# Performance work log

Measured on AMD Instinct MI355X. Metric: run time of the kernel, lower is better.

Reference implementation:

```python
import jax, jax.numpy as jnp
import numpy as np

HEAD_DIM = 64
N_HEADS = 32
N_KV_HEADS = 8
ROPE_THETA = 10000.0


def _rotate_half(x):
    h = x.shape[-1] // 2
    return jnp.concatenate([-x[..., h:], x[..., :h]], axis=-1)


def _rope_cos_sin(position_ids, head_dim, theta, dtype):
    # position_ids: [b, s] int
    inv_freq = 1.0 / (theta ** (jnp.arange(0, head_dim, 2, dtype=jnp.float32) / head_dim))
    freqs = position_ids.astype(jnp.float32)[..., None] * inv_freq  # [b, s, hd/2]
    emb = jnp.concatenate([freqs, freqs], axis=-1)                  # [b, s, hd]
    return jnp.cos(emb).astype(dtype), jnp.sin(emb).astype(dtype)


def setup_inputs() -> dict:
    key = jax.random.key(0)
    ks = jax.random.split(key, 5)
    B, S, H = 2, 2048, 2048
    KVD = N_KV_HEADS * HEAD_DIM
    x = jax.random.normal(ks[0], (B, S, H), dtype=jnp.float32)
    position_ids = jnp.broadcast_to(jnp.arange(S, dtype=jnp.int64), (B, S))
    # additive causal mask: 0 on/below diagonal, -1e9 above
    causal = jnp.triu(jnp.full((S, S), -1e9, dtype=jnp.float32), k=1)
    mask = causal[None, None, :, :]
    sc = 1.0 / np.sqrt(H)
    wq = jax.random.normal(ks[1], (H, H), dtype=jnp.float32) * sc
    wk = jax.random.normal(ks[2], (KVD, H), dtype=jnp.float32) * sc
    wv = jax.random.normal(ks[3], (KVD, H), dtype=jnp.float32) * sc
    wo = jax.random.normal(ks[4], (H, H), dtype=jnp.float32) * sc
    return {"x": x, "position_ids": position_ids, "mask": mask,
            "wq": wq, "wk": wk, "wv": wv, "wo": wo}


def reference(x, position_ids, mask, wq, wk, wv, wo):
    b, s, h = x.shape
    kv_groups = N_HEADS // N_KV_HEADS
    # projections (Linear with weight [out, in])
    xq = jnp.einsum('bsh,oh->bso', x, wq)
    xk = jnp.einsum('bsh,oh->bso', x, wk)
    xv = jnp.einsum('bsh,oh->bso', x, wv)
    q = xq.reshape(b, s, N_HEADS, HEAD_DIM).transpose(0, 2, 1, 3)      # [b,H,s,d]
    k = xk.reshape(b, s, N_KV_HEADS, HEAD_DIM).transpose(0, 2, 1, 3)   # [b,Hk,s,d]
    v = xv.reshape(b, s, N_KV_HEADS, HEAD_DIM).transpose(0, 2, 1, 3)
    cos, sin = _rope_cos_sin(position_ids, HEAD_DIM, ROPE_THETA, x.dtype)
    cos = cos[:, None, :, :]  # [b,1,s,d]
    sin = sin[:, None, :, :]
    q = q * cos + _rotate_half(q) * sin
    k = k * cos + _rotate_half(k) * sin
    # GQA expand
    k = jnp.repeat(k, kv_groups, axis=1)  # [b,H,s,d]
    v = jnp.repeat(v, kv_groups, axis=1)
    scale = 1.0 / np.sqrt(HEAD_DIM)
    attn = jnp.einsum('bhqd,bhkd->bhqk', q, k) * scale
    attn = attn + mask[:, :, :s, :s]
    attn = jax.nn.softmax(attn.astype(jnp.float32), axis=-1).astype(q.dtype)
    out = jnp.einsum('bhqk,bhkd->bhqd', attn, v)        # [b,H,s,d]
    out = out.transpose(0, 2, 1, 3).reshape(b, s, h)
    return jnp.einsum('bsh,oh->bso', out, wo)
```

## Files before the change

kernel.cpp:

```cpp
#include <hip/hip_runtime.h>

typedef __bf16 bf16;
typedef __bf16 bf16x4 __attribute__((ext_vector_type(4)));
typedef __bf16 bf16x8 __attribute__((ext_vector_type(8)));
typedef float f32x4 __attribute__((ext_vector_type(4)));

#define MFMA16(a, b, c) __builtin_amdgcn_mfma_f32_16x16x32_bf16(a, b, c, 0, 0, 0)

__device__ inline bf16x8 cvt8(const float* __restrict__ p) {
  float4 f0 = ((const float4*)p)[0];
  float4 f1 = ((const float4*)p)[1];
  bf16x8 v;
  v[0] = (bf16)f0.x; v[1] = (bf16)f0.y; v[2] = (bf16)f0.z; v[3] = (bf16)f0.w;
  v[4] = (bf16)f1.x; v[5] = (bf16)f1.y; v[6] = (bf16)f1.z; v[7] = (bf16)f1.w;
  return v;
}

__device__ inline void gl_lds16(const bf16* g, bf16* l) {
  __builtin_amdgcn_global_load_lds(
      (const __attribute__((address_space(1))) unsigned int*)g,
      (__attribute__((address_space(3))) unsigned int*)l, 16, 0, 0);
}

__global__ void detect_kernel(const unsigned* __restrict__ mask,
                              int* __restrict__ flag) {
  *flag = (mask[0] != 0u) ? 1 : 0;
}

__global__ __launch_bounds__(256) void convert_kernel(
    const void* __restrict__ s0, bf16* __restrict__ d0, int n0,
    const void* __restrict__ s1, bf16* __restrict__ d1, int n1,
    const void* __restrict__ s2, bf16* __restrict__ d2, int n2,
    const void* __restrict__ s3, bf16* __restrict__ d3, int n3,
    const int* __restrict__ flag) {
  const int isb = *flag;
  const int c0 = n0 >> 3, c1 = c0 + (n1 >> 3), c2 = c1 + (n2 >> 3);
  const int total = c2 + (n3 >> 3);
  for (int c = blockIdx.x * 256 + threadIdx.x; c < total;
       c += gridDim.x * 256) {
    const void* s; bf16* d; int off;
    if (c < c0)      { s = s0; d = d0; off = c; }
    else if (c < c1) { s = s1; d = d1; off = c - c0; }
    else if (c < c2) { s = s2; d = d2; off = c - c1; }
    else             { s = s3; d = d3; off = c - c2; }
    if (isb) ((uint4*)d)[off] = ((const uint4*)s)[off];
    else     ((bf16x8*)d)[off] = cvt8((const float*)s + (size_t)off * 8);
  }
}

template <int MODE>
__global__ __launch_bounds__(256) void gemm_bt(
    const bf16* __restrict__ Ab, const bf16* __restrict__ Wq,
    const bf16* __restrict__ Wk, const bf16* __restrict__ Wv,
    void* __restrict__ O0, bf16* __restrict__ O1, bf16* __restrict__ O2,
    const int* __restrict__ flag) {
  const int K = 2048;
  __shared__ __align__(16) bf16 As[128 * 32];
  __shared__ __align__(16) bf16 Bs[128 * 32];

  const int m0 = blockIdx.x * 128;
  const int n0 = blockIdx.y * 128;

  const bf16* W;
  int nw0;
  if (MODE == 0) {
    if (n0 < 2048) { W = Wq; nw0 = n0; }
    else if (n0 < 2560) { W = Wk; nw0 = n0 - 2048; }
    else { W = Wv; nw0 = n0 - 2560; }
  } else {
    W = Wq; nw0 = n0;
  }

  const int t = threadIdx.x;
  const int w = t >> 6, lane = t & 63, quad = lane >> 4, l15 = lane & 15;
  const int wm = (w >> 1) * 64, wn = (w & 1) * 64;

  const int ca = t, cb = t + 256;
  const bf16* ga0 = Ab + (size_t)(m0 + (ca >> 2)) * K + (ca & 3) * 8;
  const bf16* ga1 = Ab + (size_t)(m0 + (cb >> 2)) * K + (cb & 3) * 8;
  const bf16* gb0 = W + (size_t)(nw0 + (ca >> 2)) * K + (ca & 3) * 8;
  const bf16* gb1 = W + (size_t)(nw0 + (cb >> 2)) * K + (cb & 3) * 8;
  bf16* lA0 = &As[w * 512];
  bf16* lA1 = &As[2048 + w * 512];
  bf16* lB0 = &Bs[w * 512];
  bf16* lB1 = &Bs[2048 + w * 512];

  f32x4 acc[4][4] = {};

  for (int k0 = 0; k0 < K; k0 += 32) {
    __syncthreads();
    gl_lds16(ga0 + k0, lA0);
    gl_lds16(ga1 + k0, lA1);
    gl_lds16(gb0 + k0, lB0);
    gl_lds16(gb1 + k0, lB1);
    __syncthreads();

    bf16x8 a[4], b[4];
#pragma unroll
    for (int i = 0; i < 4; i++)
      a[i] = *(const bf16x8*)&As[(wm + i * 16 + l15) * 32 + quad * 8];
#pragma unroll
    for (int j = 0; j < 4; j++)
      b[j] = *(const bf16x8*)&Bs[(wn + j * 16 + l15) * 32 + quad * 8];
#pragma unroll
    for (int i = 0; i < 4; i++)
#pragma unroll
      for (int j = 0; j < 4; j++)
        acc[i][j] = MFMA16(a[i], b[j], acc[i][j]);
  }

  if (MODE == 0 && n0 >= 2560) {
#pragma unroll
    for (int i = 0; i < 4; i++)
#pragma unroll
      for (int j = 0; j < 4; j++) {
        int m = m0 + wm + i * 16 + quad * 4;
        int n = (n0 - 2560) + wn + j * 16 + l15;
        int hh = n >> 6, d = n & 63;
        int b_ = m >> 11, s = m & 2047;
        bf16x4 pv;
#pragma unroll
        for (int r = 0; r < 4; r++) pv[r] = (bf16)acc[i][j][r];
        *(bf16x4*)&O2[(((size_t)b_ * 8 + hh) * 64 + d) * 2048 + s] = pv;
      }
    return;
  }
  const int isb = (MODE == 1) ? *flag : 0;
#pragma unroll
  for (int i = 0; i < 4; i++)
#pragma unroll
    for (int j = 0; j < 4; j++)
#pragma unroll
      for (int r = 0; r < 4; r++) {
        int m = m0 + wm + i * 16 + quad * 4 + r;
        int n = n0 + wn + j * 16 + l15;
        float fv = acc[i][j][r];
        if (MODE == 1) {
          if (isb) ((bf16*)O0)[(size_t)m * 2048 + n] = (bf16)fv;
          else     ((float*)O0)[(size_t)m * 2048 + n] = fv;
        } else {
          bf16 bv = (bf16)fv;
          int b_ = m >> 11, s = m & 2047;
          if (n < 2048) {
            int h = n >> 6, d = n & 63;
            ((bf16*)O0)[(((size_t)b_ * 32 + h) * 2048 + s) * 64 + d] = bv;
          } else {
            int nn = n - 2048, h = nn >> 6, d = nn & 63;
            O1[(((size_t)b_ * 8 + h) * 2048 + s) * 64 + d] = bv;
          }
        }
      }
}

__global__ __launch_bounds__(256) void rope_table_kernel(float2* __restrict__ tab) {
  int i = blockIdx.x * 256 + threadIdx.x;
  int s = i >> 5, fi = i & 31;
  float inv = 1.0f / powf(10000.0f, (float)(2 * fi) / 64.0f);
  float fr = (float)s * inv;
  tab[i] = make_float2(cosf(fr), sinf(fr));
}

__global__ __launch_bounds__(256) void rope_kernel(bf16* __restrict__ qb,
                                                   bf16* __restrict__ kb,
                                                   const float2* __restrict__ tab,
                                                   const int* __restrict__ flag) {
  const int QROWS = 2 * 32 * 2048;
  const int isb = *flag;
  int row = blockIdx.x * 8 + (threadIdx.x >> 5);
  int d = threadIdx.x & 31;
  bf16* base = (row < QROWS) ? qb + (size_t)row * 64
                             : kb + (size_t)(row - QROWS) * 64;
  int s = row & 2047;
  float2 cs = tab[s * 32 + d];
  float cb = cs.x, sb = cs.y;
  if (isb) { cb = (float)(bf16)cb; sb = (float)(bf16)sb; }
  float v0 = (float)base[d], v1 = (float)base[d + 32];
  base[d]      = (bf16)(v0 * cb - v1 * sb);
  base[d + 32] = (bf16)(v1 * cb + v0 * sb);
}

__global__ __launch_bounds__(256) void flash_kernel(
    const bf16* __restrict__ qb, const bf16* __restrict__ kb,
    const bf16* __restrict__ vb, bf16* __restrict__ ao) {
  __shared__ __align__(16) bf16 Ks[64 * 64];
  __shared__ __align__(16) bf16 Vt[64 * 72];
  __shared__ __align__(16) bf16 Ps[4][16 * 72];

  const int bx = blockIdx.x;
  const int h = blockIdx.y;
  const int b = blockIdx.z;
  const int kvh = h >> 2;
  const int t = threadIdx.x, w = t >> 6, lane = t & 63;
  const int quad = lane >> 4, l15 = lane & 15;

  const bf16* kg = kb + ((size_t)b * 8 + kvh) * 2048 * 64;
  const bf16* vg = vb + ((size_t)b * 8 + kvh) * 64 * 2048;

  const int vd = t >> 3;
  const int vs = (t & 7) * 8;

#pragma unroll 1
  for (int ti = 0; ti < 2; ti++) {
    const int q0 = (ti == 0 ? bx : 31 - bx) * 64;
    const bf16* qg = qb + (((size_t)b * 32 + h) * 2048 + q0) * 64;

    __syncthreads();
#pragma unroll
    for (int i = 0; i < 2; i++) {
      int c = t + i * 256;
      int row = c >> 3, slot = c & 7;
      *(uint4*)&Ks[row * 64 + ((slot ^ (row & 7)) << 3)] = ((const uint4*)qg)[c];
    }
    __syncthreads();
    const int qrow = w * 16 + l15;
    bf16x8 aq0 = *(const bf16x8*)&Ks[qrow * 64 + ((quad ^ (qrow & 7)) << 3)];
    bf16x8 aq1 = *(const bf16x8*)&Ks[qrow * 64 + (((4 + quad) ^ (qrow & 7)) << 3)];

    f32x4 Oacc[4] = {};
    float m_sm = -1e30f, l_sm = 0.0f;

    const int nk = q0 + 64;
    const int qmax = q0 + w * 16 + 15;
    const int qr_sm = q0 + w * 16 + l15;

    uint4 kr0 = ((const uint4*)kg)[t];
    uint4 kr1 = ((const uint4*)kg)[t + 256];
    uint4 vr0 = *(const uint4*)(vg + (size_t)vd * 2048 + vs);
    uint4 vr1 = *(const uint4*)(vg + (size_t)(vd + 32) * 2048 + vs);

    for (int k0 = 0; k0 < nk; k0 += 64) {
      __syncthreads();
      {
        int row = t >> 3, slot = t & 7;
        *(uint4*)&Ks[row * 64 + ((slot ^ (row & 7)) << 3)] = kr0;
        int row1 = row + 32;
        *(uint4*)&Ks[row1 * 64 + ((slot ^ (row1 & 7)) << 3)] = kr1;
      }
      *(uint4*)&Vt[vd * 72 + vs] = vr0;
      *(uint4*)&Vt[(vd + 32) * 72 + vs] = vr1;
      __syncthreads();

      if (k0 + 64 < nk) {
        const bf16* kn = kg + (size_t)(k0 + 64) * 64;
        kr0 = ((const uint4*)kn)[t];
        kr1 = ((const uint4*)kn)[t + 256];
        vr0 = *(const uint4*)(vg + (size_t)vd * 2048 + (k0 + 64) + vs);
        vr1 = *(const uint4*)(vg + (size_t)(vd + 32) * 2048 + (k0 + 64) + vs);
      }

      f32x4 sf[4] = {};
#pragma unroll
      for (int sub = 0; sub < 4; sub++) {
        if (k0 + sub * 16 <= qmax) {
          int rr = sub * 16 + l15;
          bf16x8 bk0 = *(const bf16x8*)&Ks[rr * 64 + ((quad ^ (rr & 7)) << 3)];
          bf16x8 bk1 = *(const bf16x8*)&Ks[rr * 64 + (((4 + quad) ^ (rr & 7)) << 3)];
          sf[sub] = MFMA16(bk0, aq0, sf[sub]);
          sf[sub] = MFMA16(bk1, aq1, sf[sub]);
        }
      }

#pragma unroll
      for (int sub = 0; sub < 4; sub++) {
        int kk = k0 + sub * 16 + quad * 4;
#pragma unroll
        for (int r = 0; r < 4; r++) {
          float v = sf[sub][r] * 0.125f;
          sf[sub][r] = (kk + r > qr_sm) ? -1e30f : v;
        }
      }

      float mx;
      {
        f32x4 t4;
#pragma unroll
        for (int r = 0; r < 4; r++)
          t4[r] = fmaxf(fmaxf(sf[0][r], sf[1][r]), fmaxf(sf[2][r], sf[3][r]));
        mx = fmaxf(fmaxf(t4[0], t4[1]), fmaxf(t4[2], t4[3]));
      }
      mx = fmaxf(mx, __shfl_xor(mx, 16));
      mx = fmaxf(mx, __shfl_xor(mx, 32));

      float mnew = fmaxf(m_sm, mx);
      float alpha_sm = __expf(m_sm - mnew);
      m_sm = mnew;

#pragma unroll
      for (int sub = 0; sub < 4; sub++)
#pragma unroll
        for (int r = 0; r < 4; r++) sf[sub][r] = __expf(sf[sub][r] - mnew);

      float rs;
      {
        f32x4 t4;
#pragma unroll
        for (int r = 0; r < 4; r++)
          t4[r] = (sf[0][r] + sf[1][r]) + (sf[2][r] + sf[3][r]);
        rs = (t4[0] + t4[1]) + (t4[2] + t4[3]);
      }
      rs += __shfl_xor(rs, 16);
      rs += __shfl_xor(rs, 32);
      l_sm = alpha_sm * l_sm + rs;

      f32x4 alpha_pv;
#pragma unroll
      for (int r = 0; r < 4; r++) alpha_pv[r] = __shfl(alpha_sm, quad * 4 + r);
#pragma unroll
      for (int tt = 0; tt < 4; tt++)
#pragma unroll
        for (int r = 0; r < 4; r++) Oacc[tt][r] *= alpha_pv[r];

#pragma unroll
      for (int sub = 0; sub < 4; sub++) {
        bf16x4 pk;
#pragma unroll
        for (int r = 0; r < 4; r++) pk[r] = (bf16)sf[sub][r];
        *(bf16x4*)&Ps[w][l15 * 72 + sub * 16 + quad * 4] = pk;
      }
      asm volatile("s_waitcnt lgkmcnt(0)" ::: "memory");
      __builtin_amdgcn_sched_barrier(0);

      bf16x8 ap0 = *(const bf16x8*)&Ps[w][l15 * 72 + quad * 8];
#pragma unroll
      for (int tt = 0; tt < 4; tt++) {
        bf16x8 bv = *(const bf16x8*)&Vt[(tt * 16 + l15) * 72 + quad * 8];
        Oacc[tt] = MFMA16(ap0, bv, Oacc[tt]);
      }
      if (k0 + 32 <= qmax) {
        bf16x8 ap1 = *(const bf16x8*)&Ps[w][l15 * 72 + 32 + quad * 8];
#pragma unroll
        for (int tt = 0; tt < 4; tt++) {
          bf16x8 bv = *(const bf16x8*)&Vt[(tt * 16 + l15) * 72 + 32 + quad * 8];
          Oacc[tt] = MFMA16(ap1, bv, Oacc[tt]);
        }
      }
    }

    f32x4 lv;
#pragma unroll
    for (int r = 0; r < 4; r++) lv[r] = __shfl(l_sm, quad * 4 + r);
#pragma unroll
    for (int tt = 0; tt < 4; tt++)
#pragma unroll
      for (int r = 0; r < 4; r++) {
        int m = q0 + w * 16 + quad * 4 + r;
        ao[((size_t)b * 2048 + m) * 2048 + h * 64 + tt * 16 + l15] =
            (bf16)(Oacc[tt][r] / lv[r]);
      }
  }
}

extern "C" void kernel_launch(void* const* d_in, const int* in_sizes, int n_in,
                              void* d_out, int out_size, void* d_ws,
                              size_t ws_size, hipStream_t stream) {
  const void* x = d_in[0];
  const unsigned* maskw = (const unsigned*)d_in[2];
  const void* wq = d_in[3];
  const void* wk = d_in[4];
  const void* wv = d_in[5];
  const void* wo = d_in[6];

  char* ws = (char*)d_ws;
  bf16* qbuf  = (bf16*)(ws);
  bf16* kbuf  = (bf16*)(ws + 16777216);
  bf16* vbuf  = (bf16*)(ws + 20971520);
  bf16* wob   = (bf16*)(ws + 16777216);
  bf16* aobuf = (bf16*)(ws + 25165824);
  bf16* xb    = (bf16*)(ws + 25165824);
  int* flag   = (int*)(ws + 41943040);
  bf16* wqb   = (bf16*)(ws + 41943104);
  bf16* wkb   = (bf16*)(ws + 50331712);
  bf16* wvb   = (bf16*)(ws + 52428864);
  float2* rtab = (float2*)(ws + 54526016);

  detect_kernel<<<1, 1, 0, stream>>>(maskw, flag);
  rope_table_kernel<<<256, 256, 0, stream>>>(rtab);
  convert_kernel<<<2048, 256, 0, stream>>>(x, xb, 8388608, wq, wqb, 4194304,
                                           wk, wkb, 1048576, wv, wvb, 1048576,
                                           flag);
  gemm_bt<0><<<dim3(32, 24), 256, 0, stream>>>(xb, wqb, wkb, wvb, qbuf, kbuf,
                                               vbuf, flag);
  rope_kernel<<<20480, 256, 0, stream>>>(qbuf, kbuf, rtab, flag);
  flash_kernel<<<dim3(16, 32, 2), 256, 0, stream>>>(qbuf, kbuf, vbuf, aobuf);
  convert_kernel<<<2048, 256, 0, stream>>>(wo, wob, 4194304, nullptr, nullptr,
                                           0, nullptr, nullptr, 0, nullptr,
                                           nullptr, 0, flag);
  gemm_bt<1><<<dim3(32, 16), 256, 0, stream>>>(aobuf, wob, nullptr, nullptr,
                                               d_out, nullptr, nullptr, flag);
}
```

Before: 357.9 us.

## Fuse RoPE into QKV GEMM epilogue and add lazy rescaling to flash softmax

```diff
diff --git a/kernel.cpp b/kernel.cpp
--- a/kernel.cpp
+++ b/kernel.cpp
@@ -6,6 +6,7 @@
 typedef float f32x4 __attribute__((ext_vector_type(4)));
 
 #define MFMA16(a, b, c) __builtin_amdgcn_mfma_f32_16x16x32_bf16(a, b, c, 0, 0, 0)
+#define L2E 1.44269504088896340736f
 
 __device__ inline bf16x8 cvt8(const float* __restrict__ p) {
   float4 f0 = ((const float4*)p)[0];
@@ -32,12 +33,18 @@
     const void* __restrict__ s1, bf16* __restrict__ d1, int n1,
     const void* __restrict__ s2, bf16* __restrict__ d2, int n2,
     const void* __restrict__ s3, bf16* __restrict__ d3, int n3,
-    const int* __restrict__ flag) {
+    float2* __restrict__ tab, const int* __restrict__ flag) {
+  const int gid = blockIdx.x * 256 + threadIdx.x;
+  if (tab && gid < 65536) {
+    int s = gid >> 5, fi = gid & 31;
+    float inv = 1.0f / powf(10000.0f, (float)(2 * fi) / 64.0f);
+    float fr = (float)s * inv;
+    tab[gid] = make_float2(cosf(fr), sinf(fr));
+  }
   const int isb = *flag;
   const int c0 = n0 >> 3, c1 = c0 + (n1 >> 3), c2 = c1 + (n2 >> 3);
   const int total = c2 + (n3 >> 3);
-  for (int c = blockIdx.x * 256 + threadIdx.x; c < total;
-       c += gridDim.x * 256) {
+  for (int c = gid; c < total; c += gridDim.x * 256) {
     const void* s; bf16* d; int off;
     if (c < c0)      { s = s0; d = d0; off = c; }
     else if (c < c1) { s = s1; d = d1; off = c - c0; }
@@ -53,7 +60,7 @@
     const bf16* __restrict__ Ab, const bf16* __restrict__ Wq,
     const bf16* __restrict__ Wk, const bf16* __restrict__ Wv,
     void* __restrict__ O0, bf16* __restrict__ O1, bf16* __restrict__ O2,
-    const int* __restrict__ flag) {
+    const float2* __restrict__ rtab, const int* __restrict__ flag) {
   const int K = 2048;
   __shared__ __align__(16) bf16 As[128 * 32];
   __shared__ __align__(16) bf16 Bs[128 * 32];
@@ -125,7 +132,52 @@
       }
     return;
   }
-  const int isb = (MODE == 1) ? *flag : 0;
+
+  const int isb = *flag;
+
+  if (MODE == 0) {
+#pragma unroll
+    for (int i = 0; i < 4; i++) {
+      int mb = m0 + wm + i * 16 + quad * 4;
+#pragma unroll
+      for (int r = 0; r < 4; r++) {
+        int s = (mb + r) & 2047;
+#pragma unroll
+        for (int jp = 0; jp < 2; jp++) {
+          int fi = jp * 16 + l15;
+          float2 cs = rtab[s * 32 + fi];
+          float cb = cs.x, sb = cs.y;
+          if (isb) { cb = (float)(bf16)cb; sb = (float)(bf16)sb; }
+          float v0 = acc[i][jp][r], v1 = acc[i][jp + 2][r];
+          acc[i][jp][r]     = v0 * cb - v1 * sb;
+          acc[i][jp + 2][r] = v1 * cb + v0 * sb;
+        }
+      }
+    }
+    const bool isQ = (n0 < 2048);
+    const float qs = isQ ? 0.125f : 1.0f;
+#pragma unroll
+    for (int i = 0; i < 4; i++)
+#pragma unroll
+      for (int j = 0; j < 4; j++)
+#pragma unroll
+        for (int r = 0; r < 4; r++) {
+          int m = m0 + wm + i * 16 + quad * 4 + r;
+          int b_ = m >> 11, s = m & 2047;
+          bf16 bv = (bf16)(acc[i][j][r] * qs);
+          if (isQ) {
+            int n = n0 + wn + j * 16 + l15;
+            int h = n >> 6, d = n & 63;
+            ((bf16*)O0)[(((size_t)b_ * 32 + h) * 2048 + s) * 64 + d] = bv;
+          } else {
+            int nn = n0 - 2048 + wn + j * 16 + l15;
+            int h = nn >> 6, d = nn & 63;
+            O1[(((size_t)b_ * 8 + h) * 2048 + s) * 64 + d] = bv;
+          }
+        }
+    return;
+  }
+
 #pragma unroll
   for (int i = 0; i < 4; i++)
 #pragma unroll
@@ -135,48 +187,9 @@
         int m = m0 + wm + i * 16 + quad * 4 + r;
         int n = n0 + wn + j * 16 + l15;
         float fv = acc[i][j][r];
-        if (MODE == 1) {
-          if (isb) ((bf16*)O0)[(size_t)m * 2048 + n] = (bf16)fv;
-          else     ((float*)O0)[(size_t)m * 2048 + n] = fv;
-        } else {
-          bf16 bv = (bf16)fv;
-          int b_ = m >> 11, s = m & 2047;
-          if (n < 2048) {
-            int h = n >> 6, d = n & 63;
-            ((bf16*)O0)[(((size_t)b_ * 32 + h) * 2048 + s) * 64 + d] = bv;
-          } else {
-            int nn = n - 2048, h = nn >> 6, d = nn & 63;
-            O1[(((size_t)b_ * 8 + h) * 2048 + s) * 64 + d] = bv;
-          }
-        }
-      }
-}
-
-__global__ __launch_bounds__(256) void rope_table_kernel(float2* __restrict__ tab) {
-  int i = blockIdx.x * 256 + threadIdx.x;
-  int s = i >> 5, fi = i & 31;
-  float inv = 1.0f / powf(10000.0f, (float)(2 * fi) / 64.0f);
-  float fr = (float)s * inv;
-  tab[i] = make_float2(cosf(fr), sinf(fr));
-}
-
-__global__ __launch_bounds__(256) void rope_kernel(bf16* __restrict__ qb,
-                                                   bf16* __restrict__ kb,
-                                                   const float2* __restrict__ tab,
-                                                   const int* __restrict__ flag) {
-  const int QROWS = 2 * 32 * 2048;
-  const int isb = *flag;
-  int row = blockIdx.x * 8 + (threadIdx.x >> 5);
-  int d = threadIdx.x & 31;
-  bf16* base = (row < QROWS) ? qb + (size_t)row * 64
-                             : kb + (size_t)(row - QROWS) * 64;
-  int s = row & 2047;
-  float2 cs = tab[s * 32 + d];
-  float cb = cs.x, sb = cs.y;
-  if (isb) { cb = (float)(bf16)cb; sb = (float)(bf16)sb; }
-  float v0 = (float)base[d], v1 = (float)base[d + 32];
-  base[d]      = (bf16)(v0 * cb - v1 * sb);
-  base[d + 32] = (bf16)(v1 * cb + v0 * sb);
+        if (isb) ((bf16*)O0)[(size_t)m * 2048 + n] = (bf16)fv;
+        else     ((float*)O0)[(size_t)m * 2048 + n] = fv;
+      }
 }
 
 __global__ __launch_bounds__(256) void flash_kernel(
@@ -220,8 +233,9 @@
     float m_sm = -1e30f, l_sm = 0.0f;
 
     const int nk = q0 + 64;
-    const int qmax = q0 + w * 16 + 15;
-    const int qr_sm = q0 + w * 16 + l15;
+    const int qmin = q0 + w * 16;
+    const int qmax = qmin + 15;
+    const int qr_sm = qmin + l15;
 
     uint4 kr0 = ((const uint4*)kg)[t];
     uint4 kr1 = ((const uint4*)kg)[t + 256];
@@ -260,13 +274,13 @@
         }
       }
 
-#pragma unroll
-      for (int sub = 0; sub < 4; sub++) {
-        int kk = k0 + sub * 16 + quad * 4;
-#pragma unroll
-        for (int r = 0; r < 4; r++) {
-          float v = sf[sub][r] * 0.125f;
-          sf[sub][r] = (kk + r > qr_sm) ? -1e30f : v;
+      if (k0 + 64 > qmin) {
+#pragma unroll
+        for (int sub = 0; sub < 4; sub++) {
+          int kk = k0 + sub * 16 + quad * 4;
+#pragma unroll
+          for (int r = 0; r < 4; r++)
+            if (kk + r > qr_sm) sf[sub][r] = -1e30f;
         }
       }
 
@@ -281,14 +295,26 @@
       mx = fmaxf(mx, __shfl_xor(mx, 16));
       mx = fmaxf(mx, __shfl_xor(mx, 32));
 
-      float mnew = fmaxf(m_sm, mx);
-      float alpha_sm = __expf(m_sm - mnew);
-      m_sm = mnew;
-
+      if (!__all(mx <= m_sm + 8.0f)) {
+        float mnew = fmaxf(m_sm, mx);
+        float alpha = __expf(m_sm - mnew);
+        l_sm *= alpha;
+        m_sm = mnew;
+        f32x4 apv;
+#pragma unroll
+        for (int r = 0; r < 4; r++) apv[r] = __shfl(alpha, quad * 4 + r);
+#pragma unroll
+        for (int tt = 0; tt < 4; tt++)
+#pragma unroll
+          for (int r = 0; r < 4; r++) Oacc[tt][r] *= apv[r];
+      }
+
+      const float ml2 = m_sm * L2E;
 #pragma unroll
       for (int sub = 0; sub < 4; sub++)
 #pragma unroll
-        for (int r = 0; r < 4; r++) sf[sub][r] = __expf(sf[sub][r] - mnew);
+        for (int r = 0; r < 4; r++)
+          sf[sub][r] = exp2f(fmaf(sf[sub][r], L2E, -ml2));
 
       float rs;
       {
@@ -300,15 +326,7 @@
       }
       rs += __shfl_xor(rs, 16);
       rs += __shfl_xor(rs, 32);
-      l_sm = alpha_sm * l_sm + rs;
-
-      f32x4 alpha_pv;
-#pragma unroll
-      for (int r = 0; r < 4; r++) alpha_pv[r] = __shfl(alpha_sm, quad * 4 + r);
-#pragma unroll
-      for (int tt = 0; tt < 4; tt++)
-#pragma unroll
-        for (int r = 0; r < 4; r++) Oacc[tt][r] *= alpha_pv[r];
+      l_sm += rs;
 
 #pragma unroll
       for (int sub = 0; sub < 4; sub++) {
@@ -374,17 +392,16 @@
   float2* rtab = (float2*)(ws + 54526016);
 
   detect_kernel<<<1, 1, 0, stream>>>(maskw, flag);
-  rope_table_kernel<<<256, 256, 0, stream>>>(rtab);
   convert_kernel<<<2048, 256, 0, stream>>>(x, xb, 8388608, wq, wqb, 4194304,
                                            wk, wkb, 1048576, wv, wvb, 1048576,
-                                           flag);
+                                           rtab, flag);
   gemm_bt<0><<<dim3(32, 24), 256, 0, stream>>>(xb, wqb, wkb, wvb, qbuf, kbuf,
-                                               vbuf, flag);
-  rope_kernel<<<20480, 256, 0, stream>>>(qbuf, kbuf, rtab, flag);
+                                               vbuf, rtab, flag);
   flash_kernel<<<dim3(16, 32, 2), 256, 0, stream>>>(qbuf, kbuf, vbuf, aobuf);
   convert_kernel<<<2048, 256, 0, stream>>>(wo, wob, 4194304, nullptr, nullptr,
                                            0, nullptr, nullptr, 0, nullptr,
-                                           nullptr, 0, flag);
+                                           nullptr, 0, nullptr, flag);
   gemm_bt<1><<<dim3(32, 16), 256, 0, stream>>>(aobuf, wob, nullptr, nullptr,
-                                               d_out, nullptr, nullptr, flag);
-}
+                                               d_out, nullptr, nullptr, rtab,
+                                               flag);
+}
```

Result: slower. 395.8 us (+10.6%).
